# Kernel optimization log

Measured on AMD Instinct MI355X. Metric: run time of the kernel, lower is better.

Reference implementation:

```python
import jax, jax.numpy as jnp
import numpy as np

POINT_NUM = 262144
SAMPLE_NUM = 30

# Fixed obstacle polygons from the original module (ragged vertex counts)
OBSTACLES = [
    np.array([[1.23, 3.47], [1.75, 4.0], [2.1, 3.63], [1.58, 2.3], [1.4, 2.67]], dtype=np.float32),
    np.array([[4.65, 5.98], [4.0, 6.48], [4.52, 7.68], [5.06, 7.73], [5.9, 6.95]], dtype=np.float32),
    np.array([[6.78, 3.4], [7.78, 5.1], [7.78, 3.76]], dtype=np.float32),
    np.array([[4.0, 3.0], [4.35, 3.35], [4.8, 3.45], [4.37, 2.75]], dtype=np.float32),
]


def _full_path(starting, path, ending):
    # [P+1, 2] where P = point_num
    return jnp.concatenate([starting[None, :], path, ending[None, :]], axis=0)


def _collision_wzy(fullpath):
    p = fullpath[:-1]                      # [P, 2] segment origins
    r = fullpath[1:] - fullpath[:-1]       # [P, 2] segment directions
    total = jnp.asarray(0.0, fullpath.dtype)
    for ob in OBSTACLES:
        q = jnp.asarray(ob)                # [E, 2]
        s = jnp.roll(q, -1, axis=0) - q    # [E, 2] polygon edges
        qp = q[None, :, :] - p[:, None, :]                      # [P, E, 2]
        denom = r[:, 0:1] * s[None, :, 1] - r[:, 1:2] * s[None, :, 0] + 1e-8  # [P, E]
        t = (qp[..., 0] * s[None, :, 1] - qp[..., 1] * s[None, :, 0]) / denom
        u = (qp[..., 0] * r[:, None, 1] - qp[..., 1] * r[:, None, 0]) / denom
        collt = 1.0 - (t / jnp.abs(t) * (t - 1.0) / jnp.abs(t - 1.0) + 1.0) / 2.0
        collu = 1.0 - (u / jnp.abs(u) * (u - 1.0) / jnp.abs(u - 1.0) + 1.0) / 2.0
        total = total + jnp.sum(collt * collu)
    return total


def _collision_fxy(fullpath):
    p = fullpath[:-1]
    r = fullpath[1:] - fullpath[:-1]
    dt = fullpath.dtype
    # original builds [p+r, p+r*1/30, ..., p+r*29/30] -> [30*P, 2]
    fracs = jnp.concatenate([jnp.ones((1,), dt),
                             jnp.arange(1, SAMPLE_NUM, dtype=dt) / SAMPLE_NUM])
    sample = (p[None, :, :] + fracs[:, None, None] * r[None, :, :]).reshape(-1, 2)
    coll = jnp.asarray(0.0, dt)
    for ob in OBSTACLES:
        q = jnp.asarray(ob)
        s = jnp.roll(q, -1, axis=0) - q
        di = jnp.stack([s[:, 1], -s[:, 0]], axis=1)   # outward edge normals [E,2]
        di = di / jnp.linalg.norm(di, axis=1, keepdims=True)
        sq = sample[:, None, :] - q[None, :, :]       # [30P, E, 2]
        temp = jax.nn.relu(jnp.sum(sq * di[None, :, :], axis=2) + 0.1)  # [30P, E]
        coll = coll + jnp.sum(jnp.prod(temp, axis=1))
    return coll


def _lpath(fullpath):
    xp = fullpath[1:] - fullpath[:-1]
    return jnp.sum(jnp.sqrt(1e-6 + jnp.sum(xp ** 2, axis=1)))


def setup_inputs() -> dict:
    key = jax.random.key(0)
    k1, k2, k3 = jax.random.split(key, 3)
    # coordinates live in a ~10x10 planning box per the hard-coded obstacles
    path = jax.random.uniform(k1, (POINT_NUM - 1, 2), dtype=jnp.float32) * 10.0
    starting = jax.random.uniform(k2, (2,), dtype=jnp.float32) * 10.0
    ending = jax.random.uniform(k3, (2,), dtype=jnp.float32) * 10.0
    return {"path": path, "starting": starting, "ending": ending}


def reference(path, starting, ending):
    fullpath = _full_path(starting, path, ending)
    wzy = _collision_wzy(fullpath)
    fxy = _collision_fxy(fullpath)
    lp = _lpath(fullpath)
    return jnp.stack([wzy, fxy, lp])  # [3] losses
```

## Files before the change

kernel.cpp:

```cpp
#include <hip/hip_runtime.h>
#include <math.h>

#define NSEG   262144
#define NVERT  17
#define NBLK   1024

struct alignas(16) Partial { float w, f, l, pad; };

struct EdgeC { float qx, qy, sx, sy, dx, dy, c0, k; };

constexpr double csqrt_(double x) {
  double g = x > 1.0 ? x : 1.0;
  for (int i = 0; i < 64; ++i) g = 0.5 * (g + x / g);
  return g;
}
constexpr EdgeC mkedge(double qx, double qy, double nx, double ny) {
  double sx = nx - qx, sy = ny - qy;
  double n = csqrt_(sx * sx + sy * sy);
  double dx = sy / n, dy = -sx / n;
  return EdgeC{(float)qx, (float)qy, (float)sx, (float)sy,
               (float)dx, (float)dy, (float)(0.1 - (qx * dx + qy * dy)),
               (float)(qx * sy - qy * sx)};
}
constexpr EdgeC E[NVERT] = {
  mkedge(1.23,3.47, 1.75,4.0), mkedge(1.75,4.0, 2.1,3.63), mkedge(2.1,3.63, 1.58,2.3),
  mkedge(1.58,2.3, 1.4,2.67),  mkedge(1.4,2.67, 1.23,3.47),
  mkedge(4.65,5.98, 4.0,6.48), mkedge(4.0,6.48, 4.52,7.68), mkedge(4.52,7.68, 5.06,7.73),
  mkedge(5.06,7.73, 5.9,6.95), mkedge(5.9,6.95, 4.65,5.98),
  mkedge(6.78,3.4, 7.78,5.1),  mkedge(7.78,5.1, 7.78,3.76), mkedge(7.78,3.76, 6.78,3.4),
  mkedge(4.0,3.0, 4.35,3.35),  mkedge(4.35,3.35, 4.8,3.45), mkedge(4.8,3.45, 4.37,2.75),
  mkedge(4.37,2.75, 4.0,3.0)
};

struct TdTab { double v[31][6]; };
constexpr TdTab mktab() {
  TdTab t{};
  for (int m = 0; m <= 30; ++m)
    for (int j = 0; j < 6; ++j) {
      double s = 0.0;
      for (int k = 1; k <= m; ++k) {
        double f = k / 30.0, p = 1.0;
        for (int q = 0; q < j; ++q) p *= f;
        s += p;
      }
      t.v[m][j] = s;
    }
  return t;
}
__device__ constexpr TdTab TD = mktab();

__device__ __forceinline__ int imax_(int a, int b) { return a > b ? a : b; }
__device__ __forceinline__ int imin_(int a, int b) { return a < b ? a : b; }

template<int B0, int N>
__device__ __forceinline__ double obstacle_sum(const float (&A)[NVERT],
                                               const float (&Bv)[NVERT],
                                               const double (&Td)[31][6]) {
  float lo = -1e30f, hi = 1e30f;
  #pragma unroll
  for (int e = B0; e < B0 + N; ++e) {
    const float b = Bv[e];
    float inv = __builtin_amdgcn_rcpf(b);
    inv = inv * (2.0f - b * inv);
    const float fstar = -A[e] * inv;
    const bool bp = b > 0.f;
    lo = fmaxf(lo, bp ? fstar : -1e30f);
    hi = fminf(hi, bp ? 1e30f : fstar);
  }
  int k1 = (int)ceilf(lo * 30.f);
  int k2 = (int)floorf(hi * 30.f);
  k1 = imin_(imax_(k1, 1), 31);
  k2 = imin_(imax_(k2, k1 - 1), 30);
  const int m1 = k1 - 1;

  double c[N + 1];
  c[0] = (double)A[B0];
  c[1] = (double)Bv[B0];
  #pragma unroll
  for (int e = B0 + 1; e < B0 + N; ++e) {
    const double Ad = (double)A[e], Bd = (double)Bv[e];
    const int sz = e - B0 + 1;
    double prev = c[0];
    c[0] = Ad * c[0];
    #pragma unroll
    for (int j = 1; j < sz; ++j) {
      const double t = c[j];
      c[j] = fma(Ad, c[j], Bd * prev);
      prev = t;
    }
    c[sz] = Bd * prev;
  }

  double s = 0.0;
  #pragma unroll
  for (int j = 0; j <= N; ++j)
    s = fma(c[j], Td[k2][j] - Td[m1][j], s);
  return s;
}

__global__ __launch_bounds__(256)
void path_cost_kernel(const float2* __restrict__ path,
                      const float2* __restrict__ st,
                      const float2* __restrict__ en,
                      Partial* __restrict__ ws) {
  __shared__ double Td[31][6];
  if (threadIdx.x < 186)
    ((double*)Td)[threadIdx.x] = ((const double*)TD.v)[threadIdx.x];
  __syncthreads();

  const int i = blockIdx.x * 256 + threadIdx.x;

  const float2 a = (i == 0)        ? *st : path[i - 1];
  const float2 b = (i == NSEG - 1) ? *en : path[i];
  const float rx = b.x - a.x, ry = b.y - a.y;

  float lpv = sqrtf(fmaf(ry, ry, fmaf(rx, rx, 1e-6f)));

  const float c = fmaf(a.x, ry, -(a.y * rx));
  int hits = 0;
  #pragma unroll
  for (int e = 0; e < NVERT; ++e) {
    const float den = fmaf(rx, E[e].sy, fmaf(-ry, E[e].sx, 1e-8f));
    const float nt  = fmaf(-a.x, E[e].sy, fmaf(a.y, E[e].sx, E[e].k));
    const float nu  = fmaf(E[e].qx, ry, -fmaf(E[e].qy, rx, c));
    const float mn  = fminf(nt, nu);
    const float mx  = fmaxf(nt, nu);
    hits += (mn > fminf(0.f, den)) && (mx < fmaxf(0.f, den));
  }
  float wzy = (float)hits;

  float A[NVERT], B[NVERT];
  #pragma unroll
  for (int e = 0; e < NVERT; ++e) {
    A[e] = fmaf(a.x, E[e].dx, fmaf(a.y, E[e].dy, E[e].c0));
    B[e] = fmaf(rx, E[e].dx, ry * E[e].dy);
  }
  const double s0 = obstacle_sum<0, 5>(A, B, Td);
  const double s1 = obstacle_sum<5, 5>(A, B, Td);
  const double s2 = obstacle_sum<10, 3>(A, B, Td);
  const double s3 = obstacle_sum<13, 4>(A, B, Td);
  float fxy = (float)((s0 + s1) + (s2 + s3));

  #pragma unroll
  for (int o = 32; o > 0; o >>= 1) {
    wzy += __shfl_down(wzy, o);
    fxy += __shfl_down(fxy, o);
    lpv += __shfl_down(lpv, o);
  }
  __shared__ float sm[3][4];
  const int wid = threadIdx.x >> 6;
  if ((threadIdx.x & 63) == 0) { sm[0][wid] = wzy; sm[1][wid] = fxy; sm[2][wid] = lpv; }
  __syncthreads();
  if (threadIdx.x == 0) {
    Partial p;
    p.w = (sm[0][0] + sm[0][1]) + (sm[0][2] + sm[0][3]);
    p.f = (sm[1][0] + sm[1][1]) + (sm[1][2] + sm[1][3]);
    p.l = (sm[2][0] + sm[2][1]) + (sm[2][2] + sm[2][3]);
    p.pad = 0.f;
    ws[blockIdx.x] = p;
  }
}

__global__ __launch_bounds__(256)
void reduce_kernel(const Partial* __restrict__ ws, float* __restrict__ out) {
  const int t = threadIdx.x;
  float w = 0.f, f = 0.f, l = 0.f;
  #pragma unroll
  for (int j = 0; j < NBLK / 256; ++j) {
    const Partial p = ws[t + j * 256];
    w += p.w; f += p.f; l += p.l;
  }
  #pragma unroll
  for (int o = 32; o > 0; o >>= 1) {
    w += __shfl_down(w, o);
    f += __shfl_down(f, o);
    l += __shfl_down(l, o);
  }
  __shared__ float sm[3][4];
  const int wid = t >> 6;
  if ((t & 63) == 0) { sm[0][wid] = w; sm[1][wid] = f; sm[2][wid] = l; }
  __syncthreads();
  if (t == 0) {
    out[0] = (sm[0][0] + sm[0][1]) + (sm[0][2] + sm[0][3]);
    out[1] = (sm[1][0] + sm[1][1]) + (sm[1][2] + sm[1][3]);
    out[2] = (sm[2][0] + sm[2][1]) + (sm[2][2] + sm[2][3]);
  }
}

extern "C" void kernel_launch(void* const* d_in, const int* in_sizes, int n_in,
                              void* d_out, int out_size, void* d_ws, size_t ws_size,
                              hipStream_t stream) {
  (void)in_sizes; (void)n_in; (void)out_size; (void)ws_size;

  const float2* path = (const float2*)d_in[0];
  const float2* st   = (const float2*)d_in[1];
  const float2* en   = (const float2*)d_in[2];
  Partial* ws = (Partial*)d_ws;
  float* out = (float*)d_out;

  path_cost_kernel<<<NBLK, 256, 0, stream>>>(path, st, en, ws);
  reduce_kernel<<<1, 256, 0, stream>>>(ws, out);
}
```

Baseline: 12.45 us.

## Replace FP64 power-sum table with centered FP32 closed-form moment sums

The obstacle sum now expands the per-segment polynomial around the midpoint of the valid sample range. Odd central power sums vanish, so only the even terms are kept, and S0, S2 and S4 are computed in closed form. This removes the shared-memory FP64 prefix-sum table, its block-wide barrier and all double-precision multiply-adds. The work moves to FP32 with fewer terms, at the cost of some precision headroom in the product and sum compared with the previous double accumulation.

```diff
diff --git a/kernel.cpp b/kernel.cpp
--- a/kernel.cpp
+++ b/kernel.cpp
@@ -32,30 +32,12 @@
   mkedge(4.37,2.75, 4.0,3.0)
 };
 
-struct TdTab { double v[31][6]; };
-constexpr TdTab mktab() {
-  TdTab t{};
-  for (int m = 0; m <= 30; ++m)
-    for (int j = 0; j < 6; ++j) {
-      double s = 0.0;
-      for (int k = 1; k <= m; ++k) {
-        double f = k / 30.0, p = 1.0;
-        for (int q = 0; q < j; ++q) p *= f;
-        s += p;
-      }
-      t.v[m][j] = s;
-    }
-  return t;
-}
-__device__ constexpr TdTab TD = mktab();
-
 __device__ __forceinline__ int imax_(int a, int b) { return a > b ? a : b; }
 __device__ __forceinline__ int imin_(int a, int b) { return a < b ? a : b; }
 
 template<int B0, int N>
-__device__ __forceinline__ double obstacle_sum(const float (&A)[NVERT],
-                                               const float (&Bv)[NVERT],
-                                               const double (&Td)[31][6]) {
+__device__ __forceinline__ float obstacle_sum(const float (&A)[NVERT],
+                                              const float (&Bv)[NVERT]) {
   float lo = -1e30f, hi = 1e30f;
   #pragma unroll
   for (int e = B0; e < B0 + N; ++e) {
@@ -71,30 +53,35 @@
   int k2 = (int)floorf(hi * 30.f);
   k1 = imin_(imax_(k1, 1), 31);
   k2 = imin_(imax_(k2, k1 - 1), 30);
-  const int m1 = k1 - 1;
 
-  double c[N + 1];
-  c[0] = (double)A[B0];
-  c[1] = (double)Bv[B0];
+  const float fn = (float)(k2 - k1 + 1);
+  const float f0 = (float)(k1 + k2) * (1.0f / 60.0f);
+  const float n2 = fn * fn;
+  const float S0 = fn;
+  const float S2 = fn * (n2 - 1.f) * (1.f / (12.f * 900.f));
+  const float S4 = fn * (n2 - 1.f) * fmaf(3.f, n2, -7.f) * (1.f / (240.f * 810000.f));
+
+  float c[N + 1];
+  c[0] = fmaf(f0, Bv[B0], A[B0]);
+  c[1] = Bv[B0];
   #pragma unroll
   for (int e = B0 + 1; e < B0 + N; ++e) {
-    const double Ad = (double)A[e], Bd = (double)Bv[e];
+    const float Ad = fmaf(f0, Bv[e], A[e]);
+    const float Bd = Bv[e];
     const int sz = e - B0 + 1;
-    double prev = c[0];
+    float prev = c[0];
     c[0] = Ad * c[0];
     #pragma unroll
     for (int j = 1; j < sz; ++j) {
-      const double t = c[j];
-      c[j] = fma(Ad, c[j], Bd * prev);
+      const float t = c[j];
+      c[j] = fmaf(Ad, c[j], Bd * prev);
       prev = t;
     }
     c[sz] = Bd * prev;
   }
 
-  double s = 0.0;
-  #pragma unroll
-  for (int j = 0; j <= N; ++j)
-    s = fma(c[j], Td[k2][j] - Td[m1][j], s);
+  float s = fmaf(c[2], S2, c[0] * S0);
+  if constexpr (N >= 4) s = fmaf(c[4], S4, s);
   return s;
 }
 
@@ -103,11 +90,6 @@
                       const float2* __restrict__ st,
                       const float2* __restrict__ en,
                       Partial* __restrict__ ws) {
-  __shared__ double Td[31][6];
-  if (threadIdx.x < 186)
-    ((double*)Td)[threadIdx.x] = ((const double*)TD.v)[threadIdx.x];
-  __syncthreads();
-
   const int i = blockIdx.x * 256 + threadIdx.x;
 
   const float2 a = (i == 0)        ? *st : path[i - 1];
@@ -135,11 +117,8 @@
     A[e] = fmaf(a.x, E[e].dx, fmaf(a.y, E[e].dy, E[e].c0));
     B[e] = fmaf(rx, E[e].dx, ry * E[e].dy);
   }
-  const double s0 = obstacle_sum<0, 5>(A, B, Td);
-  const double s1 = obstacle_sum<5, 5>(A, B, Td);
-  const double s2 = obstacle_sum<10, 3>(A, B, Td);
-  const double s3 = obstacle_sum<13, 4>(A, B, Td);
-  float fxy = (float)((s0 + s1) + (s2 + s3));
+  float fxy = (obstacle_sum<0, 5>(A, B) + obstacle_sum<5, 5>(A, B)) +
+              (obstacle_sum<10, 3>(A, B) + obstacle_sum<13, 4>(A, B));
 
   #pragma unroll
   for (int o = 32; o > 0; o >>= 1) {
```

Result: slower. 13.01 us (+4.5%).
